# Kernel tuning notes

Hardware: AMD Instinct MI355X
Metric: run time of the kernel (lower is better)

## Reference

```python
import jax, jax.numpy as jnp
import numpy as np

DIM = 1024
HEADS = 16
HEAD_DIM = DIM // HEADS
SCALE = HEAD_DIM ** -0.5


def setup_inputs() -> dict:
    key = jax.random.key(0)
    k1, k2, k3, k4 = jax.random.split(key, 4)
    x = jax.random.normal(k1, (8, 1024, DIM), dtype=jnp.float32)
    # nn.Linear weight is [out, in]; init ~ small values
    W_qkv = jax.random.normal(k2, (3 * DIM, DIM), dtype=jnp.float32) * 0.02
    W_proj = jax.random.normal(k3, (DIM, DIM), dtype=jnp.float32) * 0.02
    b_proj = jax.random.normal(k4, (DIM,), dtype=jnp.float32) * 0.02
    return {"x": x, "W_qkv": W_qkv, "W_proj": W_proj, "b_proj": b_proj}


def reference(x, W_qkv, W_proj, b_proj):
    b, n, _ = x.shape
    h, d = HEADS, HEAD_DIM
    qkv = x @ W_qkv.T  # [b, n, 3*dim]
    # rearrange 'b n (qkv h d) -> qkv b h n d'
    qkv = qkv.reshape(b, n, 3, h, d).transpose(2, 0, 3, 1, 4)
    q, k, v = qkv[0], qkv[1], qkv[2]  # each [b, h, n, d]
    dots = jnp.einsum('bhid,bhjd->bhij', q, k) * SCALE
    attn = jax.nn.softmax(dots, axis=-1)
    out = jnp.einsum('bhij,bhjd->bhid', attn, v)
    out = out.transpose(0, 2, 1, 3).reshape(b, n, h * d)  # b n (h d)
    return out @ W_proj.T + b_proj
```

## Files before the change

kernel.cpp:

```cpp
#include <hip/hip_runtime.h>
#include <math.h>

#define DIM   1024
#define HEADS 16
#define HDIM  64
#define SEQ   1024
#define BATCH 8
#define QSCALE 0.1803368801111204f
#define LDH   72
#define ABM   128

typedef __attribute__((ext_vector_type(8)))  short          short8_t;
typedef __attribute__((ext_vector_type(8)))  unsigned short ushort8_t;
typedef __attribute__((ext_vector_type(4)))  unsigned short ushort4_t;
typedef __attribute__((ext_vector_type(4)))  float          floatx4;
typedef __attribute__((ext_vector_type(16))) float          floatx16;

__device__ __forceinline__ unsigned short f2bf(float f) {
    unsigned u = __float_as_uint(f);
    u += 0x7fffu + ((u >> 16) & 1u);
    return (unsigned short)(u >> 16);
}
__device__ __forceinline__ unsigned rnd_bf(float f) {
    unsigned u = __float_as_uint(f);
    return u + 0x7fffu + ((u >> 16) & 1u);
}
__device__ __forceinline__ float fast_exp2(float x) {
#if __has_builtin(__builtin_amdgcn_exp2f)
    return __builtin_amdgcn_exp2f(x);
#else
    return exp2f(x);
#endif
}
__device__ __forceinline__ void glds16(const unsigned short* g, unsigned short* l) {
    __builtin_amdgcn_global_load_lds(
        (const __attribute__((address_space(1))) void*)g,
        (__attribute__((address_space(3))) void*)l, 16, 0, 0);
}

__global__ __launch_bounds__(256) void cvt_bf16_all(const float* __restrict__ x,
                                                    const float* __restrict__ wqkv,
                                                    const float* __restrict__ wproj,
                                                    unsigned short* __restrict__ x_o,
                                                    unsigned short* __restrict__ wqkv_o,
                                                    unsigned short* __restrict__ wproj_o) {
    const int N8_X = BATCH * SEQ * DIM / 8;
    const int N8_WQ = 3 * DIM * DIM / 8;
    const int N8_WP = DIM * DIM / 8;
    int i = blockIdx.x * 256 + threadIdx.x;
    const float* in;
    unsigned short* out;
    if (i < N8_X)               { in = x;     out = x_o; }
    else if (i < N8_X + N8_WQ)  { i -= N8_X;  in = wqkv; out = wqkv_o; }
    else                        { i -= N8_X + N8_WQ;
                                  if (i >= N8_WP) return;
                                  in = wproj; out = wproj_o; }
    const float4* p = (const float4*)in + (size_t)i * 2;
    float4 a = p[0], b = p[1];
    ushort8_t u;
    u[0] = f2bf(a.x); u[1] = f2bf(a.y); u[2] = f2bf(a.z); u[3] = f2bf(a.w);
    u[4] = f2bf(b.x); u[5] = f2bf(b.y); u[6] = f2bf(b.z); u[7] = f2bf(b.w);
    ((ushort8_t*)out)[i] = u;
}

template<int MODE>
__global__ __launch_bounds__(256) void gemm_nt_mfma(const unsigned short* __restrict__ A,
                                                    const unsigned short* __restrict__ B,
                                                    const float* __restrict__ bias,
                                                    void* __restrict__ Cout,
                                                    unsigned short* __restrict__ vt,
                                                    int M, int N, int K) {
    __shared__ __align__(16) unsigned short As[128 * 64];
    __shared__ __align__(16) unsigned short Bs[128 * 64];

    const int tid  = threadIdx.x;
    const int lane = tid & 63;
    const int wave = tid >> 6;
    const int wm = (wave >> 1) * 64;
    const int wn = (wave & 1) * 64;
    const size_t brow = (size_t)blockIdx.x * 128;
    const size_t bcol = (size_t)blockIdx.y * 128;

    const int srow   = lane >> 3;
    const int schunk = (lane & 7) ^ srow;
    const unsigned short* gA = A + (brow + wave * 8 + srow) * (size_t)K + schunk * 8;
    const unsigned short* gB = B + (bcol + wave * 8 + srow) * (size_t)K + schunk * 8;
    unsigned short* lA = &As[wave * 512 + lane * 8];
    unsigned short* lB = &Bs[wave * 512 + lane * 8];

    floatx16 acc[2][2];
    #pragma unroll
    for (int i = 0; i < 2; i++)
        #pragma unroll
        for (int j = 0; j < 2; j++)
            #pragma unroll
            for (int r = 0; r < 16; r++) acc[i][j][r] = 0.f;

    const int c32  = lane & 31;
    const int half = lane >> 5;
    const int xr   = c32 & 7;

    for (int k0 = 0; k0 < K; k0 += 64) {
        __syncthreads();
        #pragma unroll
        for (int r = 0; r < 4; r++) {
            glds16(gA + (size_t)r * 32 * K + k0, lA + r * 2048);
            glds16(gB + (size_t)r * 32 * K + k0, lB + r * 2048);
        }
        __syncthreads();

        #pragma unroll
        for (int s = 0; s < 4; s++) {
            const int ch = ((s * 2 + half) ^ xr) * 8;
            short8_t a0 = *(const short8_t*)&As[(wm + c32) * 64 + ch];
            short8_t a1 = *(const short8_t*)&As[(wm + 32 + c32) * 64 + ch];
            short8_t b0 = *(const short8_t*)&Bs[(wn + c32) * 64 + ch];
            short8_t b1 = *(const short8_t*)&Bs[(wn + 32 + c32) * 64 + ch];
            acc[0][0] = __builtin_amdgcn_mfma_f32_32x32x16_bf16(a0, b0, acc[0][0], 0, 0, 0);
            acc[0][1] = __builtin_amdgcn_mfma_f32_32x32x16_bf16(a0, b1, acc[0][1], 0, 0, 0);
            acc[1][0] = __builtin_amdgcn_mfma_f32_32x32x16_bf16(a1, b0, acc[1][0], 0, 0, 0);
            acc[1][1] = __builtin_amdgcn_mfma_f32_32x32x16_bf16(a1, b1, acc[1][1], 0, 0, 0);
        }
    }

    if (MODE == 0) {
        #pragma unroll
        for (int mi = 0; mi < 2; mi++)
            #pragma unroll
            for (int ni = 0; ni < 2; ni++) {
                const size_t col = bcol + wn + ni * 32 + c32;
                const float bv = bias[col];
                #pragma unroll
                for (int r = 0; r < 16; r++) {
                    const size_t row = brow + wm + mi * 32 + (r & 3) + 8 * (r >> 2) + 4 * half;
                    ((float*)Cout)[row * N + col] = acc[mi][ni][r] + bv;
                }
            }
    } else {
        if (bcol < 2048) {
            const float sc = (bcol < 1024) ? QSCALE : 1.0f;
            unsigned short* qk = (unsigned short*)Cout;
            #pragma unroll
            for (int mi = 0; mi < 2; mi++)
                #pragma unroll
                for (int ni = 0; ni < 2; ni++) {
                    const size_t col = bcol + wn + ni * 32 + c32;
                    #pragma unroll
                    for (int r = 0; r < 16; r++) {
                        const size_t row = brow + wm + mi * 32 + (r & 3) + 8 * (r >> 2) + 4 * half;
                        qk[row * 2048 + col] = f2bf(acc[mi][ni][r] * sc);
                    }
                }
        } else {
            #pragma unroll
            for (int mi = 0; mi < 2; mi++)
                #pragma unroll
                for (int ni = 0; ni < 2; ni++) {
                    const int dall = (int)(bcol + wn + ni * 32 + c32) - 2048;
                    const int h = dall >> 6, d = dall & 63;
                    #pragma unroll
                    for (int rg = 0; rg < 4; rg++) {
                        const size_t row0 = brow + wm + mi * 32 + rg * 8 + 4 * half;
                        const size_t bb = row0 >> 10;
                        const int n0 = (int)(row0 & 1023);
                        ushort4_t o;
                        #pragma unroll
                        for (int q = 0; q < 4; q++) o[q] = f2bf(acc[mi][ni][rg * 4 + q]);
                        *(ushort4_t*)&vt[(((size_t)bb * HEADS + h) * HDIM + d) * SEQ + n0] = o;
                    }
                }
        }
    }
}

#define STG(t, part) do {                                                               \
    const unsigned short* g_ = (((part) < 2) ? gA0 : gB0)                               \
        + (size_t)(((part) & 1) * 128) * 1024 + (t) * 64;                               \
    unsigned short* l_ = (((part) < 2) ? lA0 : lB0)                                     \
        + ((t) & 1) * 16384 + ((part) & 1) * 8192;                                      \
    glds16(g_, l_);                                                                     \
    glds16(g_ + 64 * 1024, l_ + 4096);                                                  \
} while (0)

#define LDA(buf, mh) {                                                                  \
    const unsigned short* p_ = AsF + (buf) * 16384 + aoff + (mh) * 4096;                \
    a[0][0] = *(const short8_t*)(p_ + ch0);        a[0][1] = *(const short8_t*)(p_ + ch1); \
    a[1][0] = *(const short8_t*)(p_ + 1024 + ch0); a[1][1] = *(const short8_t*)(p_ + 1024 + ch1); \
    a[2][0] = *(const short8_t*)(p_ + 2048 + ch0); a[2][1] = *(const short8_t*)(p_ + 2048 + ch1); \
    a[3][0] = *(const short8_t*)(p_ + 3072 + ch0); a[3][1] = *(const short8_t*)(p_ + 3072 + ch1); \
}

#define LDB(buf, nh) {                                                                  \
    const unsigned short* p_ = BsF + (buf) * 16384 + boff + (nh) * 2048;                \
    b[(nh)*2+0][0] = *(const short8_t*)(p_ + ch0);        b[(nh)*2+0][1] = *(const short8_t*)(p_ + ch1); \
    b[(nh)*2+1][0] = *(const short8_t*)(p_ + 1024 + ch0); b[(nh)*2+1][1] = *(const short8_t*)(p_ + 1024 + ch1); \
}

#define MM(mh, nh) {                                                                    \
    _Pragma("unroll")                                                                   \
    for (int mf_ = 0; mf_ < 4; ++mf_) {                                                 \
        _Pragma("unroll")                                                               \
        for (int nf_ = 0; nf_ < 2; ++nf_) {                                             \
            floatx4* c_ = &acc[(mh)*4+mf_][(nh)*2+nf_];                                 \
            *c_ = __builtin_amdgcn_mfma_f32_16x16x32_bf16(a[mf_][0], b[(nh)*2+nf_][0], *c_, 0, 0, 0); \
            *c_ = __builtin_amdgcn_mfma_f32_16x16x32_bf16(a[mf_][1], b[(nh)*2+nf_][1], *c_, 0, 0, 0); \
        } } }

#define PH_TAIL(mh, nh)                                                                 \
    __builtin_amdgcn_s_barrier();                                                       \
    asm volatile("s_waitcnt lgkmcnt(0)" ::: "memory");                                  \
    __builtin_amdgcn_sched_barrier(0);                                                  \
    __builtin_amdgcn_s_setprio(1);                                                      \
    MM(mh, nh);                                                                         \
    __builtin_amdgcn_s_setprio(0);                                                      \
    __builtin_amdgcn_s_barrier();

#define VM6 asm volatile("s_waitcnt vmcnt(6)" ::: "memory")
#define VM0 asm volatile("s_waitcnt vmcnt(0)" ::: "memory")

#define GROUP(buf, S1, S2, S3, S4, VMW)                                                 \
    LDA(buf, 0); LDB(buf, 0); S1; PH_TAIL(0, 0);                                        \
    LDB(buf, 1);              S2; PH_TAIL(0, 1);                                        \
    LDA(buf, 1);              S3; PH_TAIL(1, 1);                                        \
                              S4; VMW; PH_TAIL(1, 0);

__global__ __launch_bounds__(512, 2) void gemm_qkv_8ph(const unsigned short* __restrict__ A,
                                                       const unsigned short* __restrict__ B,
                                                       unsigned short* __restrict__ qk,
                                                       unsigned short* __restrict__ vt) {
    __shared__ __align__(16) unsigned short As[2][16384];
    __shared__ __align__(16) unsigned short Bs[2][16384];

    const int tid  = threadIdx.x;
    const int lane = tid & 63;
    const int wave = tid >> 6;
    const int wm   = wave >> 2;
    const int wn   = wave & 3;
    const size_t brow = (size_t)blockIdx.x * 256;
    const size_t bcol = (size_t)blockIdx.y * 256;

    const int ro  = tid >> 3;
    const int lch = (tid & 7) ^ (ro & 7);
    const unsigned short* gA0 = A + (brow + ro) * 1024 + lch * 8;
    const unsigned short* gB0 = B + (bcol + ro) * 1024 + lch * 8;
    unsigned short* lA0 = &As[0][0] + tid * 8;
    unsigned short* lB0 = &Bs[0][0] + tid * 8;

    const int l15  = lane & 15;
    const int ch0  = (((lane >> 4)    ) ^ (lane & 7)) * 8;
    const int ch1  = (((lane >> 4) + 4) ^ (lane & 7)) * 8;
    const int aoff = (wm * 128 + l15) * 64;
    const int boff = (wn * 64  + l15) * 64;
    const unsigned short* AsF = &As[0][0];
    const unsigned short* BsF = &Bs[0][0];

    short8_t a[4][2];
    short8_t b[4][2];
    floatx4  acc[8][4];
    #pragma unroll
    for (int i = 0; i < 8; i++)
        #pragma unroll
        for (int j = 0; j < 4; j++)
            #pragma unroll
            for (int r = 0; r < 4; r++) acc[i][j][r] = 0.f;

    STG(0, 3); STG(0, 0); STG(0, 1); STG(0, 2);
    STG(1, 3); STG(1, 0); STG(1, 1);
    VM6;
    __builtin_amdgcn_s_barrier();

    #pragma unroll 1
    for (int i = 0; i < 7; ++i) {
        GROUP(0, STG(2*i+1, 2), STG(2*i+2, 3), STG(2*i+2, 0), STG(2*i+2, 1), VM6);
        GROUP(1, STG(2*i+2, 2), STG(2*i+3, 3), STG(2*i+3, 0), STG(2*i+3, 1), VM6);
    }
    GROUP(0, STG(15, 2), (void)0, (void)0, (void)0, VM0);
    GROUP(1, (void)0,    (void)0, (void)0, (void)0, (void)0);

    const int rq = (lane >> 4) << 2;
    if (bcol < 2048) {
        const float sc = (bcol < 1024) ? QSCALE : 1.0f;
        #pragma unroll
        for (int mf = 0; mf < 8; ++mf) {
            const size_t row0 = brow + wm * 128 + mf * 16 + rq;
            #pragma unroll
            for (int nf = 0; nf < 4; ++nf) {
                const size_t col = bcol + wn * 64 + nf * 16 + l15;
                #pragma unroll
                for (int q = 0; q < 4; ++q)
                    qk[(row0 + q) * 2048 + col] = f2bf(acc[mf][nf][q] * sc);
            }
        }
    } else {
        #pragma unroll
        for (int mf = 0; mf < 8; ++mf) {
            const int row0 = (int)brow + wm * 128 + mf * 16 + rq;
            const int bb = row0 >> 10, n0 = row0 & 1023;
            #pragma unroll
            for (int nf = 0; nf < 4; ++nf) {
                const int dall = (int)bcol - 2048 + wn * 64 + nf * 16 + l15;
                const int h = dall >> 6, d = dall & 63;
                ushort4_t o;
                #pragma unroll
                for (int q = 0; q < 4; ++q) o[q] = f2bf(acc[mf][nf][q]);
                *(ushort4_t*)&vt[(((size_t)bb * HEADS + h) * HDIM + d) * SEQ + n0] = o;
            }
        }
    }
}

#undef STG
#undef LDA
#undef LDB
#undef MM
#undef PH_TAIL
#undef VM6
#undef VM0
#undef GROUP

__global__ __launch_bounds__(256) void attn_mfma(const unsigned short* __restrict__ qk,
                                                 const unsigned short* __restrict__ vt,
                                                 unsigned short* __restrict__ aout) {
    const int bh = blockIdx.x;
    const int qt = blockIdx.y;
    const int h  = bh & 15;
    const int b  = bh >> 4;
    const int tid  = threadIdx.x;
    const int lane = tid & 63;
    const int wave = tid >> 6;
    const int c32  = lane & 31;
    const int half = lane >> 5;

    __shared__ __align__(16) unsigned short Qs[ABM * LDH];
    __shared__ __align__(16) unsigned short Ks[2][64 * 64];
    __shared__ __align__(16) unsigned short Vs[2][64 * 64];
    __shared__ float scr[4][32];

    const int sr = tid >> 2;
    const int sq = tid & 3;
    const int sx = sr & 7;
    const unsigned short* ksrc0 =
        qk + ((size_t)(b * SEQ + sr)) * 2048 + DIM + h * HDIM + sq * 16;
    const unsigned short* vsrc0 =
        vt + (((size_t)(b * HEADS + h)) * HDIM + sr) * SEQ + sq * 16;
    const int kvo0 = sr * 64 + (((sq * 2)     ^ sx) * 8);
    const int kvo1 = sr * 64 + (((sq * 2 + 1) ^ sx) * 8);

    ushort8_t ck0 = *(const ushort8_t*)ksrc0;
    ushort8_t ck1 = *(const ushort8_t*)(ksrc0 + 8);
    ushort8_t cv0 = *(const ushort8_t*)vsrc0;
    ushort8_t cv1 = *(const ushort8_t*)(vsrc0 + 8);

    {
        const int r  = tid >> 1;
        const int c0 = (tid & 1) * 32;
        const unsigned short* src =
            qk + ((size_t)(b * SEQ + qt * ABM + r)) * 2048 + h * HDIM + c0;
        unsigned short* dst = &Qs[r * LDH + c0];
        *(ushort8_t*)(dst)      = *(const ushort8_t*)(src);
        *(ushort8_t*)(dst + 8)  = *(const ushort8_t*)(src + 8);
        *(ushort8_t*)(dst + 16) = *(const ushort8_t*)(src + 16);
        *(ushort8_t*)(dst + 24) = *(const ushort8_t*)(src + 24);
    }
    __syncthreads();

    short8_t bq[4];
    #pragma unroll
    for (int s = 0; s < 4; s++)
        bq[s] = *(const short8_t*)&Qs[(wave * 32 + c32) * LDH + s * 16 + half * 8];

    floatx16 O[2];
    #pragma unroll
    for (int dt = 0; dt < 2; dt++)
        #pragma unroll
        for (int r = 0; r < 16; r++) O[dt][r] = 0.f;
    float lsum = 0.f;

    const int fxr = c32 & 7;

    for (int kt = 0; kt < SEQ / 64; kt++) {
        const int cur = kt & 1;
        *(ushort8_t*)&Ks[cur][kvo0] = ck0;
        *(ushort8_t*)&Ks[cur][kvo1] = ck1;
        *(ushort8_t*)&Vs[cur][kvo0] = cv0;
        *(ushort8_t*)&Vs[cur][kvo1] = cv1;
        __syncthreads();
        if (kt + 1 < SEQ / 64) {
            const unsigned short* ks = ksrc0 + (size_t)(kt + 1) * 64 * 2048;
            const unsigned short* vs = vsrc0 + (kt + 1) * 64;
            ck0 = *(const ushort8_t*)ks;
            ck1 = *(const ushort8_t*)(ks + 8);
            cv0 = *(const ushort8_t*)vs;
            cv1 = *(const ushort8_t*)(vs + 8);
        }

        floatx16 S[2];
        #pragma unroll
        for (int t = 0; t < 2; t++)
            #pragma unroll
            for (int r = 0; r < 16; r++) S[t][r] = 0.f;
        #pragma unroll
        for (int t = 0; t < 2; t++)
            #pragma unroll
            for (int s = 0; s < 4; s++) {
                const int slot = ((s * 2 + half) ^ fxr) * 8;
                short8_t ak = *(const short8_t*)&Ks[cur][(t * 32 + c32) * 64 + slot];
                S[t] = __builtin_amdgcn_mfma_f32_32x32x16_bf16(ak, bq[s], S[t], 0, 0, 0);
            }

        #pragma unroll
        for (int t = 0; t < 2; t++)
            #pragma unroll
            for (int rg = 0; rg < 4; rg++) {
                const float p0 = fast_exp2(S[t][rg * 4 + 0]);
                const float p1 = fast_exp2(S[t][rg * 4 + 1]);
                const float p2 = fast_exp2(S[t][rg * 4 + 2]);
                const float p3 = fast_exp2(S[t][rg * 4 + 3]);
                lsum += (p0 + p1) + (p2 + p3);
                const unsigned r01 = __builtin_amdgcn_perm(rnd_bf(p1), rnd_bf(p0), 0x07060302);
                const unsigned r23 = __builtin_amdgcn_perm(rnd_bf(p3), rnd_bf(p2), 0x07060302);
                *(uint2*)&Qs[(wave * 32 + c32) * LDH + t * 32 + rg * 8 + 4 * half] =
                    make_uint2(r01, r23);
            }

        short8_t ap[4];
        #pragma unroll
        for (int s = 0; s < 4; s++)
            ap[s] = *(const short8_t*)&Qs[(wave * 32 + c32) * LDH + s * 16 + half * 8];
        #pragma unroll
        for (int dt = 0; dt < 2; dt++)
            #pragma unroll
            for (int s = 0; s < 4; s++) {
                const int slot = ((s * 2 + half) ^ fxr) * 8;
                short8_t bv = *(const short8_t*)&Vs[cur][(dt * 32 + c32) * 64 + slot];
                O[dt] = __builtin_amdgcn_mfma_f32_32x32x16_bf16(ap[s], bv, O[dt], 0, 0, 0);
            }
    }

    lsum += __shfl_xor(lsum, 32);
    if (half == 0) scr[wave][c32] = 1.0f / lsum;
    __builtin_amdgcn_s_waitcnt(0);

    #pragma unroll
    for (int rg = 0; rg < 4; rg++) {
        const float4 inv4 = *(const float4*)&scr[wave][rg * 8 + 4 * half];
        #pragma unroll
        for (int q = 0; q < 4; q++) {
            const float invl = ((const float*)&inv4)[q];
            const size_t row = (size_t)b * SEQ + qt * ABM + wave * 32 + rg * 8 + 4 * half + q;
            #pragma unroll
            for (int dt = 0; dt < 2; dt++)
                aout[row * DIM + h * HDIM + dt * 32 + c32] = f2bf(O[dt][rg * 4 + q] * invl);
        }
    }
}

extern "C" void kernel_launch(void* const* d_in, const int* in_sizes, int n_in,
                              void* d_out, int out_size, void* d_ws, size_t ws_size,
                              hipStream_t stream) {
    const float* x      = (const float*)d_in[0];
    const float* W_qkv  = (const float*)d_in[1];
    const float* W_proj = (const float*)d_in[2];
    const float* b_proj = (const float*)d_in[3];
    float* out = (float*)d_out;

    const int M = BATCH * SEQ;

    unsigned short* ws       = (unsigned short*)d_ws;
    unsigned short* x_bf     = ws;
    unsigned short* wqkv_bf  = x_bf + (size_t)M * DIM;
    unsigned short* wproj_bf = wqkv_bf + (size_t)3 * DIM * DIM;
    unsigned short* qk_bf    = wproj_bf + (size_t)DIM * DIM;
    unsigned short* vt_bf    = qk_bf + (size_t)M * 2048;
    unsigned short* aout_bf  = vt_bf + (size_t)BATCH * HEADS * HDIM * SEQ;

    {
        const int n8 = (M * DIM + 3 * DIM * DIM + DIM * DIM) / 8;
        cvt_bf16_all<<<(n8 + 255) / 256, 256, 0, stream>>>(
            x, W_qkv, W_proj, x_bf, wqkv_bf, wproj_bf);
    }

    gemm_qkv_8ph<<<dim3(M / 256, 3 * DIM / 256), 512, 0, stream>>>(
        x_bf, wqkv_bf, qk_bf, vt_bf);

    attn_mfma<<<dim3(BATCH * HEADS, SEQ / ABM), 256, 0, stream>>>(qk_bf, vt_bf, aout_bf);

    gemm_nt_mfma<0><<<dim3(M / 128, DIM / 128), 256, 0, stream>>>(
        aout_bf, wproj_bf, b_proj, out, nullptr, M, DIM, DIM);
}
```

Baseline: 238.3 us.

## Add XCD-aware block swizzle and prefetch next-buffer B fragment in QKV GEMM

Both GEMM kernels now remap block indices so that blocks dispatched to the same XCD cover a contiguous 2D region of the output. The goal is better L2 reuse of the A and B tiles. In the 8-phase QKV GEMM, the first B fragment load of the next LDS buffer moves to the end of the previous group's last phase, right after its MFMAs. This lets that LDS read overlap the barrier instead of sitting at the start of the group. The swizzle assumes grid dimensions divisible by 4 and 2, and the early LDS read adds register pressure and depends on the stage data already being visible.

```diff
diff --git a/kernel.cpp b/kernel.cpp
--- a/kernel.cpp
+++ b/kernel.cpp
@@ -36,6 +36,15 @@
     __builtin_amdgcn_global_load_lds(
         (const __attribute__((address_space(1))) void*)g,
         (__attribute__((address_space(3))) void*)l, 16, 0, 0);
+}
+
+__device__ __forceinline__ void xcd_swizzle(int& bx, int& by) {
+    const int lin = blockIdx.y * gridDim.x + blockIdx.x;
+    const int cw  = gridDim.x >> 2;
+    const int chh = gridDim.y >> 1;
+    const int i   = lin >> 3;
+    bx = (lin & 3) * cw + i / chh;
+    by = ((lin >> 2) & 1) * chh + i % chh;
 }
 
 __global__ __launch_bounds__(256) void cvt_bf16_all(const float* __restrict__ x,
@@ -78,8 +87,10 @@
     const int wave = tid >> 6;
     const int wm = (wave >> 1) * 64;
     const int wn = (wave & 1) * 64;
-    const size_t brow = (size_t)blockIdx.x * 128;
-    const size_t bcol = (size_t)blockIdx.y * 128;
+    int bxi, byi;
+    xcd_swizzle(bxi, byi);
+    const size_t brow = (size_t)bxi * 128;
+    const size_t bcol = (size_t)byi * 128;
 
     const int srow   = lane >> 3;
     const int schunk = (lane & 7) ^ srow;
@@ -215,14 +226,24 @@
     __builtin_amdgcn_s_setprio(0);                                                      \
     __builtin_amdgcn_s_barrier();
 
+#define PH_TAIL_NB(mh, nh, NB)                                                          \
+    __builtin_amdgcn_s_barrier();                                                       \
+    asm volatile("s_waitcnt lgkmcnt(0)" ::: "memory");                                  \
+    __builtin_amdgcn_sched_barrier(0);                                                  \
+    __builtin_amdgcn_s_setprio(1);                                                      \
+    MM(mh, nh);                                                                         \
+    __builtin_amdgcn_s_setprio(0);                                                      \
+    NB;                                                                                 \
+    __builtin_amdgcn_s_barrier();
+
 #define VM6 asm volatile("s_waitcnt vmcnt(6)" ::: "memory")
 #define VM0 asm volatile("s_waitcnt vmcnt(0)" ::: "memory")
 
-#define GROUP(buf, S1, S2, S3, S4, VMW)                                                 \
-    LDA(buf, 0); LDB(buf, 0); S1; PH_TAIL(0, 0);                                        \
-    LDB(buf, 1);              S2; PH_TAIL(0, 1);                                        \
-    LDA(buf, 1);              S3; PH_TAIL(1, 1);                                        \
-                              S4; VMW; PH_TAIL(1, 0);
+#define GROUP(buf, S1, S2, S3, S4, VMW, NB)                                             \
+    LDA(buf, 0); S1; PH_TAIL(0, 0);                                                     \
+    LDB(buf, 1); S2; PH_TAIL(0, 1);                                                     \
+    LDA(buf, 1); S3; PH_TAIL(1, 1);                                                     \
+                 S4; VMW; PH_TAIL_NB(1, 0, NB);
 
 __global__ __launch_bounds__(512, 2) void gemm_qkv_8ph(const unsigned short* __restrict__ A,
                                                        const unsigned short* __restrict__ B,
@@ -236,8 +257,10 @@
     const int wave = tid >> 6;
     const int wm   = wave >> 2;
     const int wn   = wave & 3;
-    const size_t brow = (size_t)blockIdx.x * 256;
-    const size_t bcol = (size_t)blockIdx.y * 256;
+    int bxi, byi;
+    xcd_swizzle(bxi, byi);
+    const size_t brow = (size_t)bxi * 256;
+    const size_t bcol = (size_t)byi * 256;
 
     const int ro  = tid >> 3;
     const int lch = (tid & 7) ^ (ro & 7);
@@ -268,14 +291,15 @@
     STG(1, 3); STG(1, 0); STG(1, 1);
     VM6;
     __builtin_amdgcn_s_barrier();
+    LDB(0, 0);
 
     #pragma unroll 1
     for (int i = 0; i < 7; ++i) {
-        GROUP(0, STG(2*i+1, 2), STG(2*i+2, 3), STG(2*i+2, 0), STG(2*i+2, 1), VM6);
-        GROUP(1, STG(2*i+2, 2), STG(2*i+3, 3), STG(2*i+3, 0), STG(2*i+3, 1), VM6);
-    }
-    GROUP(0, STG(15, 2), (void)0, (void)0, (void)0, VM0);
-    GROUP(1, (void)0,    (void)0, (void)0, (void)0, (void)0);
+        GROUP(0, STG(2*i+1, 2), STG(2*i+2, 3), STG(2*i+2, 0), STG(2*i+2, 1), VM6, LDB(1, 0));
+        GROUP(1, STG(2*i+2, 2), STG(2*i+3, 3), STG(2*i+3, 0), STG(2*i+3, 1), VM6, LDB(0, 0));
+    }
+    GROUP(0, STG(15, 2), (void)0, (void)0, (void)0, VM0,     LDB(1, 0));
+    GROUP(1, (void)0,    (void)0, (void)0, (void)0, (void)0, (void)0);
 
     const int rq = (lane >> 4) << 2;
     if (bcol < 2048) {
@@ -314,6 +338,7 @@
 #undef LDB
 #undef MM
 #undef PH_TAIL
+#undef PH_TAIL_NB
 #undef VM6
 #undef VM0
 #undef GROUP
```

After: 234.5 us. Within noise of the previous version (-1.6%).
